# Performance work log

Measured on AMD Instinct MI355X. Metric: run time of the kernel, lower is better.

Reference implementation:

```python
import jax, jax.numpy as jnp
import numpy as np

TEMPERATURE = 1.0
BIG = 1e30  # sentinel for masked min/max
NEG = -1e30  # masked logit


def _masked_log_softmax(x, m):
    # m: bool mask [B, N]; rows with no valid entries are handled by the caller
    return jax.nn.log_softmax(jnp.where(m, x, NEG), axis=-1)


def setup_inputs() -> dict:
    key = jax.random.key(0)
    k1, k2, k3 = jax.random.split(key, 3)
    B, N = 4096, 6000
    y_pred = jax.random.normal(k1, (B, N), dtype=jnp.float32)
    y_true = jax.random.normal(k2, (B, N), dtype=jnp.float32) * 0.05  # daily returns scale
    masks = jax.random.randint(k3, (B, N), 0, 2, dtype=jnp.int32)
    return {"y_pred": y_pred, "y_true": y_true, "masks": masks}


def reference(y_pred, y_true, masks):
    m = masks > 0  # [B, N] bool
    mf = m.astype(y_pred.dtype)
    n = mf.sum(-1)  # [B] number of valid stocks per day
    valid = n >= 2  # rows with <2 valid entries are skipped (contribute 0)

    # min-max normalize y_true over valid entries (label_smoothing == 0)
    t_min = jnp.min(jnp.where(m, y_true, BIG), axis=-1, keepdims=True)
    t_max = jnp.max(jnp.where(m, y_true, -BIG), axis=-1, keepdims=True)
    rng = t_max - t_min
    true_norm = jnp.where(rng > 0, (y_true - t_min) / (rng + 1e-12), y_true)

    logp_pred = _masked_log_softmax(y_pred / TEMPERATURE, m)
    logp_true = _masked_log_softmax(true_norm / TEMPERATURE, m)
    p_true = jnp.exp(logp_true)

    # F.kl_div(pred_prob.log(), true_prob, reduction='batchmean') on a 1-D
    # vector of length n divides the summed KL by n.
    kl_elem = jnp.where(m, p_true * (logp_true - logp_pred), 0.0)
    kl = kl_elem.sum(-1) / jnp.maximum(n, 1.0)  # [B]

    batch_size = y_pred.shape[0]
    return jnp.sum(jnp.where(valid, kl, 0.0)) / batch_size
```

## Files before the change

### kernel.cpp

```cpp
#include <hip/hip_runtime.h>
#include <math.h>

#define NCOL  6000
#define NV    1500
#define BLOCK 512
#define NWAVE 8
#define EPT   3

__device__ __forceinline__ float wave_max_f(float v) {
    #pragma unroll
    for (int off = 32; off > 0; off >>= 1) v = fmaxf(v, __shfl_xor(v, off, 64));
    return v;
}
__device__ __forceinline__ float wave_min_f(float v) {
    #pragma unroll
    for (int off = 32; off > 0; off >>= 1) v = fminf(v, __shfl_xor(v, off, 64));
    return v;
}
__device__ __forceinline__ int wave_sum_i(int v) {
    #pragma unroll
    for (int off = 32; off > 0; off >>= 1) v += __shfl_xor(v, off, 64);
    return v;
}
__device__ __forceinline__ double wave_sum_d(double v) {
    #pragma unroll
    for (int off = 32; off > 0; off >>= 1) v += __shfl_xor(v, off, 64);
    return v;
}

__global__ __launch_bounds__(BLOCK, 8) void row_kl_kernel(
    const float* __restrict__ yp, const float* __restrict__ yt,
    const int* __restrict__ mk, float* __restrict__ rowkl)
{
    __shared__ float  swf[3][NWAVE];
    __shared__ int    swi[NWAVE];
    __shared__ double swd[3][NWAVE];

    const int row  = blockIdx.x;
    const int tid  = threadIdx.x;
    const int lane = tid & 63;
    const int wid  = tid >> 6;

    const float4* yp4 = reinterpret_cast<const float4*>(yp) + (size_t)row * NV;
    const float4* yt4 = reinterpret_cast<const float4*>(yt) + (size_t)row * NV;
    const int4*   mk4 = reinterpret_cast<const int4*>(mk) + (size_t)row * NV;

    const int v2 = tid + 2 * BLOCK;
    const int vc2 = (v2 < NV) ? v2 : 0;
    float4 xp[EPT], xt[EPT];
    int4   mm[EPT];
    xp[0] = yp4[tid];
    xp[1] = yp4[tid + BLOCK];
    xp[2] = yp4[vc2];
    xt[0] = yt4[tid];
    xt[1] = yt4[tid + BLOCK];
    xt[2] = yt4[vc2];
    mm[0] = mk4[tid];
    mm[1] = mk4[tid + BLOCK];
    mm[2] = mk4[vc2];
    if (v2 >= NV) { mm[2].x = 0; mm[2].y = 0; mm[2].z = 0; mm[2].w = 0; }

    float maxp = -1e30f, tmin = 1e30f, tmax = -1e30f;
    int cnt = 0;
    #pragma unroll
    for (int j = 0; j < EPT; ++j) {
        {
            bool m = mm[j].x > 0;
            float x = m ? xp[j].x : -1e30f;
            float t = m ? xt[j].x : -1e30f;
            tmin = fminf(tmin, m ? xt[j].x : 1e30f);
            xp[j].x = x; xt[j].x = t;
            maxp = fmaxf(maxp, x); tmax = fmaxf(tmax, t); cnt += m;
        }
        {
            bool m = mm[j].y > 0;
            float x = m ? xp[j].y : -1e30f;
            float t = m ? xt[j].y : -1e30f;
            tmin = fminf(tmin, m ? xt[j].y : 1e30f);
            xp[j].y = x; xt[j].y = t;
            maxp = fmaxf(maxp, x); tmax = fmaxf(tmax, t); cnt += m;
        }
        {
            bool m = mm[j].z > 0;
            float x = m ? xp[j].z : -1e30f;
            float t = m ? xt[j].z : -1e30f;
            tmin = fminf(tmin, m ? xt[j].z : 1e30f);
            xp[j].z = x; xt[j].z = t;
            maxp = fmaxf(maxp, x); tmax = fmaxf(tmax, t); cnt += m;
        }
        {
            bool m = mm[j].w > 0;
            float x = m ? xp[j].w : -1e30f;
            float t = m ? xt[j].w : -1e30f;
            tmin = fminf(tmin, m ? xt[j].w : 1e30f);
            xp[j].w = x; xt[j].w = t;
            maxp = fmaxf(maxp, x); tmax = fmaxf(tmax, t); cnt += m;
        }
    }

    maxp = wave_max_f(maxp);
    tmin = wave_min_f(tmin);
    tmax = wave_max_f(tmax);
    cnt  = wave_sum_i(cnt);
    if (lane == 0) { swf[0][wid] = maxp; swf[1][wid] = tmin; swf[2][wid] = tmax; swi[wid] = cnt; }
    __syncthreads();
    maxp = -1e30f; tmin = 1e30f; tmax = -1e30f; cnt = 0;
    #pragma unroll
    for (int j = 0; j < NWAVE; ++j) {
        maxp = fmaxf(maxp, swf[0][j]);
        tmin = fminf(tmin, swf[1][j]);
        tmax = fmaxf(tmax, swf[2][j]);
        cnt += swi[j];
    }

    const float rng   = tmax - tmin;
    const bool scaled = rng > 0.0f;
    const float inv_s = 1.0f / (rng + 1e-12f);
    const float maxz  = scaled ? rng * inv_s : tmax;

    double Zp = 0.0, S1 = 0.0, S2 = 0.0;
    #pragma unroll
    for (int j = 0; j < EPT; ++j) {
        #pragma unroll
        for (int c = 0; c < 4; ++c) {
            float x = (c == 0) ? xp[j].x : (c == 1) ? xp[j].y : (c == 2) ? xp[j].z : xp[j].w;
            float t = (c == 0) ? xt[j].x : (c == 1) ? xt[j].y : (c == 2) ? xt[j].z : xt[j].w;
            float ep = __expf(x - maxp);
            float z  = scaled ? (t - tmin) * inv_s : t;
            z = fmaxf(z, -1e30f);
            float e1 = __expf(z - maxz);
            Zp += (double)ep;
            S1 += (double)e1;
            S2 += (double)e1 * (double)(z - x);
        }
    }
    Zp = wave_sum_d(Zp);
    S1 = wave_sum_d(S1);
    S2 = wave_sum_d(S2);
    if (lane == 0) { swd[0][wid] = Zp; swd[1][wid] = S1; swd[2][wid] = S2; }
    __syncthreads();
    if (tid == 0) {
        double zp = 0.0, s1 = 0.0, s2 = 0.0;
        #pragma unroll
        for (int j = 0; j < NWAVE; ++j) { zp += swd[0][j]; s1 += swd[1][j]; s2 += swd[2][j]; }
        float val = 0.0f;
        if (cnt >= 2) {
            double kl = s2 / s1 + ((double)maxp + log(zp) - (double)maxz - log(s1));
            double v  = kl / (double)cnt;
            if (isfinite(v)) val = (float)v;
        }
        rowkl[row] = val;
    }
}

__global__ __launch_bounds__(256) void final_reduce_kernel(
    const float* __restrict__ rowkl, float* __restrict__ out, int nrows)
{
    __shared__ double swd[4];
    const int tid  = threadIdx.x;
    const int lane = tid & 63;
    const int wid  = tid >> 6;
    double acc = 0.0;
    for (int i = tid; i < nrows; i += 256) acc += (double)rowkl[i];
    acc = wave_sum_d(acc);
    if (lane == 0) swd[wid] = acc;
    __syncthreads();
    if (tid == 0) {
        double tot = 0.0;
        #pragma unroll
        for (int j = 0; j < 4; ++j) tot += swd[j];
        out[0] = (float)(tot / (double)nrows);
    }
}

extern "C" void kernel_launch(void* const* d_in, const int* in_sizes, int n_in,
                              void* d_out, int out_size, void* d_ws, size_t ws_size,
                              hipStream_t stream) {
    const float* y_pred = (const float*)d_in[0];
    const float* y_true = (const float*)d_in[1];
    const int*   masks  = (const int*)d_in[2];
    float* out = (float*)d_out;
    float* rowkl = (float*)d_ws;

    const int B = in_sizes[0] / NCOL;

    row_kl_kernel<<<B, BLOCK, 0, stream>>>(y_pred, y_true, masks, rowkl);
    final_reduce_kernel<<<1, 256, 0, stream>>>(rowkl, out, B);
}
```

Before: 56.95 us.

## Stage row loads through LDS via global_load_lds with 1024-thread blocks

Switches each row's block from 512 to 1024 threads and loads the pred, true and mask vectors with direct global-to-LDS async loads instead of register loads, then reads them back from shared memory. The goal is to raise memory-level parallelism and drop the third partial load per thread. In exchange it uses about 72KB of LDS per block, which limits occupancy to one or two blocks per CU. It also relies on the launch_bounds occupancy hint, now set for 1024 threads.

After: 84.21 us. 47.9% more time.

```diff
diff --git a/kernel.cpp b/kernel.cpp
--- a/kernel.cpp
+++ b/kernel.cpp
@@ -3,9 +3,15 @@
 
 #define NCOL  6000
 #define NV    1500
-#define BLOCK 512
-#define NWAVE 8
-#define EPT   3
+#define BLOCK 1024
+#define NWAVE 16
+#define SLOTS 1536
+
+__device__ __forceinline__ void gload16(const void* g, void* l) {
+    __builtin_amdgcn_global_load_lds(
+        (const __attribute__((address_space(1))) void*)g,
+        (__attribute__((address_space(3))) void*)l, 16, 0, 0);
+}
 
 __device__ __forceinline__ float wave_max_f(float v) {
     #pragma unroll
@@ -32,6 +38,9 @@
     const float* __restrict__ yp, const float* __restrict__ yt,
     const int* __restrict__ mk, float* __restrict__ rowkl)
 {
+    __shared__ float4 sp4s[SLOTS];
+    __shared__ float4 st4s[SLOTS];
+    __shared__ int4   sm4s[SLOTS];
     __shared__ float  swf[3][NWAVE];
     __shared__ int    swi[NWAVE];
     __shared__ double swd[3][NWAVE];
@@ -45,55 +54,62 @@
     const float4* yt4 = reinterpret_cast<const float4*>(yt) + (size_t)row * NV;
     const int4*   mk4 = reinterpret_cast<const int4*>(mk) + (size_t)row * NV;
 
-    const int v2 = tid + 2 * BLOCK;
-    const int vc2 = (v2 < NV) ? v2 : 0;
-    float4 xp[EPT], xt[EPT];
-    int4   mm[EPT];
-    xp[0] = yp4[tid];
-    xp[1] = yp4[tid + BLOCK];
-    xp[2] = yp4[vc2];
-    xt[0] = yt4[tid];
-    xt[1] = yt4[tid + BLOCK];
-    xt[2] = yt4[vc2];
-    mm[0] = mk4[tid];
-    mm[1] = mk4[tid + BLOCK];
-    mm[2] = mk4[vc2];
-    if (v2 >= NV) { mm[2].x = 0; mm[2].y = 0; mm[2].z = 0; mm[2].w = 0; }
-
+    {
+        const int base = wid * 64;
+        gload16(yp4 + tid, (char*)sp4s + (size_t)base * 16);
+        gload16(yt4 + tid, (char*)st4s + (size_t)base * 16);
+        gload16(mk4 + tid, (char*)sm4s + (size_t)base * 16);
+    }
+    {
+        const int base = 1024 + wid * 64;
+        if (base < NV) {
+            const int v1 = 1024 + tid;
+            const int c1 = (v1 < NV) ? v1 : (NV - 1);
+            gload16(yp4 + c1, (char*)sp4s + (size_t)base * 16);
+            gload16(yt4 + c1, (char*)st4s + (size_t)base * 16);
+            gload16(mk4 + c1, (char*)sm4s + (size_t)base * 16);
+        }
+    }
+    asm volatile("s_waitcnt vmcnt(0)" ::: "memory");
+
+    float xr[8], tr[8];
     float maxp = -1e30f, tmin = 1e30f, tmax = -1e30f;
     int cnt = 0;
-    #pragma unroll
-    for (int j = 0; j < EPT; ++j) {
-        {
-            bool m = mm[j].x > 0;
-            float x = m ? xp[j].x : -1e30f;
-            float t = m ? xt[j].x : -1e30f;
-            tmin = fminf(tmin, m ? xt[j].x : 1e30f);
-            xp[j].x = x; xt[j].x = t;
-            maxp = fmaxf(maxp, x); tmax = fmaxf(tmax, t); cnt += m;
-        }
-        {
-            bool m = mm[j].y > 0;
-            float x = m ? xp[j].y : -1e30f;
-            float t = m ? xt[j].y : -1e30f;
-            tmin = fminf(tmin, m ? xt[j].y : 1e30f);
-            xp[j].y = x; xt[j].y = t;
-            maxp = fmaxf(maxp, x); tmax = fmaxf(tmax, t); cnt += m;
-        }
-        {
-            bool m = mm[j].z > 0;
-            float x = m ? xp[j].z : -1e30f;
-            float t = m ? xt[j].z : -1e30f;
-            tmin = fminf(tmin, m ? xt[j].z : 1e30f);
-            xp[j].z = x; xt[j].z = t;
-            maxp = fmaxf(maxp, x); tmax = fmaxf(tmax, t); cnt += m;
-        }
-        {
-            bool m = mm[j].w > 0;
-            float x = m ? xp[j].w : -1e30f;
-            float t = m ? xt[j].w : -1e30f;
-            tmin = fminf(tmin, m ? xt[j].w : 1e30f);
-            xp[j].w = x; xt[j].w = t;
+
+    #pragma unroll
+    for (int b = 0; b < 2; ++b) {
+        const int v  = b * 1024 + tid;
+        const int vc = (v < NV) ? v : 0;
+        float4 xq = sp4s[vc];
+        float4 tq = st4s[vc];
+        int4   mq = sm4s[vc];
+        if (v >= NV) { mq.x = 0; mq.y = 0; mq.z = 0; mq.w = 0; }
+        {
+            bool m = mq.x > 0;
+            float x = m ? xq.x : -1e30f; float t = m ? tq.x : -1e30f;
+            tmin = fminf(tmin, m ? tq.x : 1e30f);
+            xr[4*b+0] = x; tr[4*b+0] = t;
+            maxp = fmaxf(maxp, x); tmax = fmaxf(tmax, t); cnt += m;
+        }
+        {
+            bool m = mq.y > 0;
+            float x = m ? xq.y : -1e30f; float t = m ? tq.y : -1e30f;
+            tmin = fminf(tmin, m ? tq.y : 1e30f);
+            xr[4*b+1] = x; tr[4*b+1] = t;
+            maxp = fmaxf(maxp, x); tmax = fmaxf(tmax, t); cnt += m;
+        }
+        {
+            bool m = mq.z > 0;
+            float x = m ? xq.z : -1e30f; float t = m ? tq.z : -1e30f;
+            tmin = fminf(tmin, m ? tq.z : 1e30f);
+            xr[4*b+2] = x; tr[4*b+2] = t;
+            maxp = fmaxf(maxp, x); tmax = fmaxf(tmax, t); cnt += m;
+        }
+        {
+            bool m = mq.w > 0;
+            float x = m ? xq.w : -1e30f; float t = m ? tq.w : -1e30f;
+            tmin = fminf(tmin, m ? tq.w : 1e30f);
+            xr[4*b+3] = x; tr[4*b+3] = t;
             maxp = fmaxf(maxp, x); tmax = fmaxf(tmax, t); cnt += m;
         }
     }
@@ -120,19 +136,16 @@
 
     double Zp = 0.0, S1 = 0.0, S2 = 0.0;
     #pragma unroll
-    for (int j = 0; j < EPT; ++j) {
-        #pragma unroll
-        for (int c = 0; c < 4; ++c) {
-            float x = (c == 0) ? xp[j].x : (c == 1) ? xp[j].y : (c == 2) ? xp[j].z : xp[j].w;
-            float t = (c == 0) ? xt[j].x : (c == 1) ? xt[j].y : (c == 2) ? xt[j].z : xt[j].w;
-            float ep = __expf(x - maxp);
-            float z  = scaled ? (t - tmin) * inv_s : t;
-            z = fmaxf(z, -1e30f);
-            float e1 = __expf(z - maxz);
-            Zp += (double)ep;
-            S1 += (double)e1;
-            S2 += (double)e1 * (double)(z - x);
-        }
+    for (int e = 0; e < 8; ++e) {
+        float x = xr[e];
+        float t = tr[e];
+        float ep = __expf(x - maxp);
+        float z  = scaled ? (t - tmin) * inv_s : t;
+        z = fmaxf(z, -1e30f);
+        float e1 = __expf(z - maxz);
+        Zp += (double)ep;
+        S1 += (double)e1;
+        S2 += (double)e1 * (double)(z - x);
     }
     Zp = wave_sum_d(Zp);
     S1 = wave_sum_d(S1);
```
